# Kernel tuning notes

Measured on AMD Instinct MI355X. Metric: run time of the kernel, lower is better.

Reference implementation:

```python
import jax, jax.numpy as jnp
import numpy as np

E, H, I, B, K = 8, 2048, 5632, 1024, 2


def setup_inputs() -> dict:
    key = jax.random.key(0)
    k_x, k_id, k_w, k_g, k_u, k_d = jax.random.split(key, 6)
    x = jax.random.normal(k_x, (B, H), dtype=jnp.float32)
    expert_ids = jax.random.randint(k_id, (B, K), 0, E).astype(jnp.int32)
    ew = jax.random.uniform(k_w, (B, K), dtype=jnp.float32)
    expert_weights = ew / jnp.sum(ew, axis=-1, keepdims=True)  # router probs, sum to 1
    scale = 0.02
    gate_weights = jax.random.normal(k_g, (E, H, I), dtype=jnp.float32) * scale
    up_weights = jax.random.normal(k_u, (E, H, I), dtype=jnp.float32) * scale
    down_weights = jax.random.normal(k_d, (E, I, H), dtype=jnp.float32) * scale
    return {
        "x": x,
        "expert_ids": expert_ids,
        "expert_weights": expert_weights,
        "gate_weights": gate_weights,
        "up_weights": up_weights,
        "down_weights": down_weights,
    }


def reference(x, expert_ids, expert_weights, gate_weights, up_weights, down_weights):
    # Faithful math: per token t, expert e = expert_ids[t,k]:
    #   out[t] = sum_k expert_weights[t,k] * (silu(x W_gate_e) * (x W_up_e)) W_down_e
    # Implemented as dense all-expert GEMMs + select, which computes the
    # identical per-expert matmuls as the original's gathered-weight einsums
    # without materializing the [B,K,H,I] gathered weight tensor.
    gate_all = jnp.einsum('bh,ehi->bei', x, gate_weights)        # [B,E,I]
    up_all = jnp.einsum('bh,ehi->bei', x, up_weights)            # [B,E,I]
    act_all = jax.nn.silu(gate_all) * up_all                     # [B,E,I]
    out_all = jnp.einsum('bei,eih->beh', act_all, down_weights)  # [B,E,H]
    # Select the top_k experts' outputs per token: [B,K,H]
    sel = jnp.take_along_axis(out_all, expert_ids[:, :, None], axis=1)
    return jnp.sum(sel * expert_weights[:, :, None], axis=1)     # [B,H]
```

## Files before the change

### kernel.cpp

```cpp
#include <hip/hip_runtime.h>
#include <hip/hip_bf16.h>

#define E_ 8
#define H_ 2048
#define I_ 5632
#define B_ 1024
#define K_ 2
#define NROWS (B_*K_)

#define BM 128
#define BN 64
#define BK 64
#define MAXT 24
#define NKG (H_/BK)
#define NKD (I_/BK)
#define NYG (I_/BN)
#define NYD (H_/BN)

typedef __attribute__((ext_vector_type(8))) __bf16 bf16x8;
typedef __attribute__((ext_vector_type(4))) float f32x4;

union BF4 { __bf16 b[4]; uint2 q; };
union BF8 { __bf16 b[8]; uint4 q; };

__device__ __forceinline__ void gld_lds16(const void* g, void* l) {
  __builtin_amdgcn_global_load_lds(
      (const __attribute__((address_space(1))) void*)g,
      (__attribute__((address_space(3))) void*)l, 16, 0, 0);
}

#define GLOAD4(dst, ptr) asm volatile("global_load_dwordx4 %0, %1, off" : "=v"(dst) : "v"(ptr))
#define WAITV(N) do { asm volatile("s_waitcnt vmcnt(" #N ")" ::: "memory"); __builtin_amdgcn_sched_barrier(0); } while(0)
#define WAITL()  do { asm volatile("s_waitcnt lgkmcnt(0)" ::: "memory"); __builtin_amdgcn_sched_barrier(0); } while(0)
#define BAR()    __builtin_amdgcn_s_barrier()

#define MSK(c) (((c)&7) ^ (((c)>>2)&7))

__global__ void cvtx_kernel(const float* __restrict__ x, __bf16* __restrict__ xb) {
  int i = (blockIdx.x * 256 + threadIdx.x) * 8;
  float4 a = *(const float4*)(x + i);
  float4 b = *(const float4*)(x + i + 4);
  BF8 r;
  r.b[0] = (__bf16)a.x; r.b[1] = (__bf16)a.y; r.b[2] = (__bf16)a.z; r.b[3] = (__bf16)a.w;
  r.b[4] = (__bf16)b.x; r.b[5] = (__bf16)b.y; r.b[6] = (__bf16)b.z; r.b[7] = (__bf16)b.w;
  *(uint4*)(xb + i) = r.q;
}

__global__ void route_kernel(const int* __restrict__ ids,
                             int* __restrict__ counts, int* __restrict__ offsets,
                             int* __restrict__ tlist, int* __restrict__ row_of,
                             int* __restrict__ tile_e, int* __restrict__ tile_m) {
  __shared__ int sc[E_], sp[E_], so[E_];
  int t = threadIdx.x;
  if (t < E_) { sc[t] = 0; sp[t] = 0; }
  __syncthreads();
  for (int idx = t; idx < NROWS; idx += 256) atomicAdd(&sc[ids[idx]], 1);
  __syncthreads();
  if (t == 0) {
    int acc = 0;
    for (int e = 0; e < E_; ++e) { so[e] = acc; acc += sc[e]; }
    int nt = 0;
    for (int e = 0; e < E_; ++e)
      for (int m0 = 0; m0 < sc[e]; m0 += BM) { tile_e[nt] = e; tile_m[nt] = m0; ++nt; }
    for (; nt < MAXT; ++nt) { tile_e[nt] = 0; tile_m[nt] = 0x7FFFFFFF; }
  }
  __syncthreads();
  for (int idx = t; idx < NROWS; idx += 256) {
    int e = ids[idx];
    int slot = atomicAdd(&sp[e], 1);
    int row = so[e] + slot;
    tlist[row] = idx / K_;
    row_of[idx] = row;
  }
  if (t < E_) { counts[t] = sc[t]; offsets[t] = so[t]; }
}

__global__ __launch_bounds__(256, 3) void gateup_kernel(
    const __bf16* __restrict__ xb, const float* __restrict__ gw,
    const float* __restrict__ uw, const int* __restrict__ counts,
    const int* __restrict__ offsets, const int* __restrict__ tlist,
    const int* __restrict__ tile_e, const int* __restrict__ tile_m,
    __bf16* __restrict__ act)
{
  extern __shared__ char smem[];
  char* As0 = smem;
  char* As1 = smem + 16384;
  char* Bg  = smem + 32768;
  char* Bu  = smem + 40960;

  const int id = blockIdx.x;
  const int w  = (id & 7) * 264 + (id >> 3);
  const int tt = w % MAXT;
  const int ny = w / MAXT;
  const int e  = tile_e[tt];
  const int m0 = tile_m[tt];
  const int cnt = counts[e];
  if (m0 >= cnt) return;
  const int off = offsets[e];
  const int n0 = ny * BN;

  const int tid  = threadIdx.x;
  const int lane = tid & 63;
  const int wave = tid >> 6;
  const int wr = (wave >> 1) * 64;
  const int wc = (wave & 1) * 32;

  const __bf16* asrc0; const __bf16* asrc1; const __bf16* asrc2; const __bf16* asrc3;
  int ad0, ad1, ad2, ad3;
  {
    const __bf16* s[4]; int d[4];
#pragma unroll
    for (int i = 0; i < 4; ++i) {
      int f = i*256 + tid;
      int r = f >> 3, cs = f & 7;
      int rr = m0 + r; if (rr >= cnt) rr = cnt - 1;
      int tok = tlist[off + rr];
      s[i] = xb + (size_t)tok * H_ + ((cs ^ (r & 7)) << 3);
      d[i] = f * 16;
    }
    asrc0=s[0]; asrc1=s[1]; asrc2=s[2]; asrc3=s[3];
    ad0=d[0]; ad1=d[1]; ad2=d[2]; ad3=d[3];
  }

  const int cq = tid & 15;
  const int kb = (tid >> 4) * 4;
  const float* pg0 = gw + ((size_t)e*H_ + kb + 0)*I_ + n0 + 4*cq;
  const float* pg1 = gw + ((size_t)e*H_ + kb + 1)*I_ + n0 + 4*cq;
  const float* pg2 = gw + ((size_t)e*H_ + kb + 2)*I_ + n0 + 4*cq;
  const float* pg3 = gw + ((size_t)e*H_ + kb + 3)*I_ + n0 + 4*cq;
  const float* pu0 = uw + ((size_t)e*H_ + kb + 0)*I_ + n0 + 4*cq;
  const float* pu1 = uw + ((size_t)e*H_ + kb + 1)*I_ + n0 + 4*cq;
  const float* pu2 = uw + ((size_t)e*H_ + kb + 2)*I_ + n0 + 4*cq;
  const float* pu3 = uw + ((size_t)e*H_ + kb + 3)*I_ + n0 + 4*cq;
  const int slot = kb >> 3;
  const int half = (kb & 4) << 1;
  int bw0, bw1, bw2, bw3;
  {
    int b[4];
#pragma unroll
    for (int i = 0; i < 4; ++i) {
      int c = 4*cq + i;
      b[i] = c*128 + ((slot ^ MSK(c)) << 4) + half;
    }
    bw0=b[0]; bw1=b[1]; bw2=b[2]; bw3=b[3];
  }

  f32x4 vg_0,vg_1,vg_2,vg_3, vu_0,vu_1,vu_2,vu_3;

  f32x4 accg[4][2], accu[4][2];
#pragma unroll
  for (int i = 0; i < 4; ++i)
#pragma unroll
    for (int j = 0; j < 2; ++j) {
      accg[i][j] = (f32x4){0.f,0.f,0.f,0.f};
      accu[i][j] = (f32x4){0.f,0.f,0.f,0.f};
    }

  auto COMPUTE = [&](const char* Ab) {
    __builtin_amdgcn_s_setprio(1);
#pragma unroll
    for (int kk = 0; kk < 2; ++kk) {
      const int ks = kk*4 + (lane >> 4);
      const int r0 = wr + (lane & 15);
      const int swa = (ks ^ (r0 & 7)) << 4;
      bf16x8 a0 = *(const bf16x8*)(Ab + (r0 +  0)*128 + swa);
      bf16x8 a1 = *(const bf16x8*)(Ab + (r0 + 16)*128 + swa);
      bf16x8 a2 = *(const bf16x8*)(Ab + (r0 + 32)*128 + swa);
      bf16x8 a3 = *(const bf16x8*)(Ab + (r0 + 48)*128 + swa);
      const int c0 = wc + (lane & 15);
      const int swb0 = (ks ^ MSK(c0)) << 4;
      const int swb1 = swb0 ^ (4 << 4);
      bf16x8 g0 = *(const bf16x8*)(Bg + c0*128 + swb0);
      bf16x8 g1 = *(const bf16x8*)(Bg + (c0+16)*128 + swb1);
      bf16x8 u0 = *(const bf16x8*)(Bu + c0*128 + swb0);
      bf16x8 u1 = *(const bf16x8*)(Bu + (c0+16)*128 + swb1);
      accg[0][0] = __builtin_amdgcn_mfma_f32_16x16x32_bf16(a0, g0, accg[0][0], 0,0,0);
      accg[1][0] = __builtin_amdgcn_mfma_f32_16x16x32_bf16(a1, g0, accg[1][0], 0,0,0);
      accg[2][0] = __builtin_amdgcn_mfma_f32_16x16x32_bf16(a2, g0, accg[2][0], 0,0,0);
      accg[3][0] = __builtin_amdgcn_mfma_f32_16x16x32_bf16(a3, g0, accg[3][0], 0,0,0);
      accg[0][1] = __builtin_amdgcn_mfma_f32_16x16x32_bf16(a0, g1, accg[0][1], 0,0,0);
      accg[1][1] = __builtin_amdgcn_mfma_f32_16x16x32_bf16(a1, g1, accg[1][1], 0,0,0);
      accg[2][1] = __builtin_amdgcn_mfma_f32_16x16x32_bf16(a2, g1, accg[2][1], 0,0,0);
      accg[3][1] = __builtin_amdgcn_mfma_f32_16x16x32_bf16(a3, g1, accg[3][1], 0,0,0);
      accu[0][0] = __builtin_amdgcn_mfma_f32_16x16x32_bf16(a0, u0, accu[0][0], 0,0,0);
      accu[1][0] = __builtin_amdgcn_mfma_f32_16x16x32_bf16(a1, u0, accu[1][0], 0,0,0);
      accu[2][0] = __builtin_amdgcn_mfma_f32_16x16x32_bf16(a2, u0, accu[2][0], 0,0,0);
      accu[3][0] = __builtin_amdgcn_mfma_f32_16x16x32_bf16(a3, u0, accu[3][0], 0,0,0);
      accu[0][1] = __builtin_amdgcn_mfma_f32_16x16x32_bf16(a0, u1, accu[0][1], 0,0,0);
      accu[1][1] = __builtin_amdgcn_mfma_f32_16x16x32_bf16(a1, u1, accu[1][1], 0,0,0);
      accu[2][1] = __builtin_amdgcn_mfma_f32_16x16x32_bf16(a2, u1, accu[2][1], 0,0,0);
      accu[3][1] = __builtin_amdgcn_mfma_f32_16x16x32_bf16(a3, u1, accu[3][1], 0,0,0);
    }
    __builtin_amdgcn_s_setprio(0);
  };

#define GU_PF(KPF) do { size_t o_ = (size_t)(KPF)*(size_t)BK*(size_t)I_; \
    GLOAD4(vg_0, pg0+o_); GLOAD4(vu_0, pu0+o_); \
    GLOAD4(vg_1, pg1+o_); GLOAD4(vu_1, pu1+o_); \
    GLOAD4(vg_2, pg2+o_); GLOAD4(vu_2, pu2+o_); \
    GLOAD4(vg_3, pg3+o_); GLOAD4(vu_3, pu3+o_); } while(0)

#define GU_CVW1(BB, V0, V1, V2, V3, BWI, I) do { BF4 p_; \
    p_.b[0]=(__bf16)V0[I]; p_.b[1]=(__bf16)V1[I]; p_.b[2]=(__bf16)V2[I]; p_.b[3]=(__bf16)V3[I]; \
    *(uint2*)((BB)+BWI) = p_.q; } while(0)

#define GU_CVW() do { \
    GU_CVW1(Bg, vg_0, vg_1, vg_2, vg_3, bw0, 0); \
    GU_CVW1(Bg, vg_0, vg_1, vg_2, vg_3, bw1, 1); \
    GU_CVW1(Bg, vg_0, vg_1, vg_2, vg_3, bw2, 2); \
    GU_CVW1(Bg, vg_0, vg_1, vg_2, vg_3, bw3, 3); \
    GU_CVW1(Bu, vu_0, vu_1, vu_2, vu_3, bw0, 0); \
    GU_CVW1(Bu, vu_0, vu_1, vu_2, vu_3, bw1, 1); \
    GU_CVW1(Bu, vu_0, vu_1, vu_2, vu_3, bw2, 2); \
    GU_CVW1(Bu, vu_0, vu_1, vu_2, vu_3, bw3, 3); } while(0)

#define GU_GLDA(DST, KPF) do { size_t k_ = (size_t)(KPF)*(size_t)BK; \
    gld_lds16(asrc0 + k_, (DST)+ad0); gld_lds16(asrc1 + k_, (DST)+ad1); \
    gld_lds16(asrc2 + k_, (DST)+ad2); gld_lds16(asrc3 + k_, (DST)+ad3); } while(0)

  GU_PF(0);
  WAITV(0);
  GU_CVW();
  GU_GLDA(As0, 0);
  WAITV(0);
  GU_PF(1);
  GU_GLDA(As1, 1);
  WAITL();
  BAR();

#pragma unroll 1
  for (int kt = 0; kt < NKG; kt += 2) {
    {
      int kpf = kt + 2; if (kpf > NKG-1) kpf = NKG-1;
      COMPUTE(As0);
      WAITV(4);
      WAITL();
      BAR();
      GU_CVW();
      GU_PF(kpf);
      WAITV(8);
      WAITL();
      BAR();
      GU_GLDA(As0, kpf);
    }
    {
      int kpf = kt + 3; if (kpf > NKG-1) kpf = NKG-1;
      COMPUTE(As1);
      WAITV(4);
      WAITL();
      BAR();
      GU_CVW();
      GU_PF(kpf);
      WAITV(8);
      WAITL();
      BAR();
      GU_GLDA(As1, kpf);
    }
  }
  WAITV(0);
  WAITL();

  const int rsub = (lane >> 4) * 4;
  const int csub = lane & 15;
#pragma unroll
  for (int mi = 0; mi < 4; ++mi)
#pragma unroll
    for (int j = 0; j < 4; ++j) {
      int rl = wr + mi*16 + rsub + j;
      if (m0 + rl < cnt) {
        size_t orow = (size_t)(off + m0 + rl) * I_ + n0 + wc + csub;
#pragma unroll
        for (int cg = 0; cg < 2; ++cg) {
          float g = accg[mi][cg][j];
          float u = accu[mi][cg][j];
          float sg = g / (1.0f + __expf(-g));
          act[orow + cg*16] = (__bf16)(sg * u);
        }
      }
    }
#undef GU_PF
#undef GU_CVW
#undef GU_CVW1
#undef GU_GLDA
}

__global__ __launch_bounds__(256, 3) void down_kernel(
    const __bf16* __restrict__ act, const float* __restrict__ dw,
    const int* __restrict__ counts, const int* __restrict__ offsets,
    const int* __restrict__ tile_e, const int* __restrict__ tile_m,
    float* __restrict__ rowbuf)
{
  extern __shared__ char smem[];
  char* As0 = smem;
  char* As1 = smem + 16384;
  char* Bs0 = smem + 32768;
  char* Bs1 = smem + 40960;

  const int id = blockIdx.x;
  const int w  = (id & 7) * 96 + (id >> 3);
  const int tt = w % MAXT;
  const int ny = w / MAXT;
  const int e  = tile_e[tt];
  const int m0 = tile_m[tt];
  const int cnt = counts[e];
  if (m0 >= cnt) return;
  const int off = offsets[e];
  const int n0 = ny * BN;

  const int tid  = threadIdx.x;
  const int lane = tid & 63;
  const int wave = tid >> 6;
  const int wr = (wave >> 1) * 64;
  const int wc = (wave & 1) * 32;

  const __bf16* asrc0; const __bf16* asrc1; const __bf16* asrc2; const __bf16* asrc3;
  int ad0, ad1, ad2, ad3;
  {
    const __bf16* s[4]; int d[4];
#pragma unroll
    for (int i = 0; i < 4; ++i) {
      int f = i*256 + tid;
      int r = f >> 3, cs = f & 7;
      int rr = m0 + r; if (rr >= cnt) rr = cnt - 1;
      s[i] = act + (size_t)(off + rr) * I_ + ((cs ^ (r & 7)) << 3);
      d[i] = f * 16;
    }
    asrc0=s[0]; asrc1=s[1]; asrc2=s[2]; asrc3=s[3];
    ad0=d[0]; ad1=d[1]; ad2=d[2]; ad3=d[3];
  }

  const int cq = tid & 15;
  const int kb = (tid >> 4) * 4;
  const float* pd0 = dw + ((size_t)e*I_ + kb + 0)*H_ + n0 + 4*cq;
  const float* pd1 = dw + ((size_t)e*I_ + kb + 1)*H_ + n0 + 4*cq;
  const float* pd2 = dw + ((size_t)e*I_ + kb + 2)*H_ + n0 + 4*cq;
  const float* pd3 = dw + ((size_t)e*I_ + kb + 3)*H_ + n0 + 4*cq;
  const int slot = kb >> 3;
  const int half = (kb & 4) << 1;
  int bw0, bw1, bw2, bw3;
  {
    int b[4];
#pragma unroll
    for (int i = 0; i < 4; ++i) {
      int c = 4*cq + i;
      b[i] = c*128 + ((slot ^ MSK(c)) << 4) + half;
    }
    bw0=b[0]; bw1=b[1]; bw2=b[2]; bw3=b[3];
  }

  f32x4 vdA_0,vdA_1,vdA_2,vdA_3;
  f32x4 vdB_0,vdB_1,vdB_2,vdB_3;

  f32x4 acc[4][2];
#pragma unroll
  for (int i = 0; i < 4; ++i)
#pragma unroll
    for (int j = 0; j < 2; ++j) acc[i][j] = (f32x4){0.f,0.f,0.f,0.f};

  auto COMPUTE = [&](const char* Ab, const char* Bb) {
    __builtin_amdgcn_s_setprio(1);
#pragma unroll
    for (int kk = 0; kk < 2; ++kk) {
      const int ks = kk*4 + (lane >> 4);
      const int r0 = wr + (lane & 15);
      const int swa = (ks ^ (r0 & 7)) << 4;
      bf16x8 a0 = *(const bf16x8*)(Ab + (r0 +  0)*128 + swa);
      bf16x8 a1 = *(const bf16x8*)(Ab + (r0 + 16)*128 + swa);
      bf16x8 a2 = *(const bf16x8*)(Ab + (r0 + 32)*128 + swa);
      bf16x8 a3 = *(const bf16x8*)(Ab + (r0 + 48)*128 + swa);
      const int c0 = wc + (lane & 15);
      const int swb0 = (ks ^ MSK(c0)) << 4;
      const int swb1 = swb0 ^ (4 << 4);
      bf16x8 b0 = *(const bf16x8*)(Bb + c0*128 + swb0);
      bf16x8 b1 = *(const bf16x8*)(Bb + (c0+16)*128 + swb1);
      acc[0][0] = __builtin_amdgcn_mfma_f32_16x16x32_bf16(a0, b0, acc[0][0], 0,0,0);
      acc[1][0] = __builtin_amdgcn_mfma_f32_16x16x32_bf16(a1, b0, acc[1][0], 0,0,0);
      acc[2][0] = __builtin_amdgcn_mfma_f32_16x16x32_bf16(a2, b0, acc[2][0], 0,0,0);
      acc[3][0] = __builtin_amdgcn_mfma_f32_16x16x32_bf16(a3, b0, acc[3][0], 0,0,0);
      acc[0][1] = __builtin_amdgcn_mfma_f32_16x16x32_bf16(a0, b1, acc[0][1], 0,0,0);
      acc[1][1] = __builtin_amdgcn_mfma_f32_16x16x32_bf16(a1, b1, acc[1][1], 0,0,0);
      acc[2][1] = __builtin_amdgcn_mfma_f32_16x16x32_bf16(a2, b1, acc[2][1], 0,0,0);
      acc[3][1] = __builtin_amdgcn_mfma_f32_16x16x32_bf16(a3, b1, acc[3][1], 0,0,0);
    }
    __builtin_amdgcn_s_setprio(0);
  };

#define DN_PF(S, KPF) do { size_t o_ = (size_t)(KPF)*(size_t)BK*(size_t)H_; \
    GLOAD4(vd##S##_0, pd0+o_); GLOAD4(vd##S##_1, pd1+o_); \
    GLOAD4(vd##S##_2, pd2+o_); GLOAD4(vd##S##_3, pd3+o_); } while(0)

#define DN_CVW1(BB, V0, V1, V2, V3, BWI, I) do { BF4 p_; \
    p_.b[0]=(__bf16)V0[I]; p_.b[1]=(__bf16)V1[I]; p_.b[2]=(__bf16)V2[I]; p_.b[3]=(__bf16)V3[I]; \
    *(uint2*)((BB)+BWI) = p_.q; } while(0)

#define DN_CVW(S, BB) do { \
    DN_CVW1(BB, vd##S##_0, vd##S##_1, vd##S##_2, vd##S##_3, bw0, 0); \
    DN_CVW1(BB, vd##S##_0, vd##S##_1, vd##S##_2, vd##S##_3, bw1, 1); \
    DN_CVW1(BB, vd##S##_0, vd##S##_1, vd##S##_2, vd##S##_3, bw2, 2); \
    DN_CVW1(BB, vd##S##_0, vd##S##_1, vd##S##_2, vd##S##_3, bw3, 3); } while(0)

#define DN_GLDA(DST, KPF) do { size_t k_ = (size_t)(KPF)*(size_t)BK; \
    gld_lds16(asrc0 + k_, (DST)+ad0); gld_lds16(asrc1 + k_, (DST)+ad1); \
    gld_lds16(asrc2 + k_, (DST)+ad2); gld_lds16(asrc3 + k_, (DST)+ad3); } while(0)

  DN_PF(A, 0);
  DN_GLDA(As0, 0);
  WAITV(4);
  DN_CVW(A, Bs0);
  DN_PF(B, 1);
  DN_GLDA(As1, 1);
  WAITV(8);
  WAITL();
  BAR();

#pragma unroll 1
  for (int kt = 0; kt < NKD; kt += 2) {
    {
      int kpf = kt + 2; if (kpf > NKD-1) kpf = NKD-1;
      DN_PF(A, kpf);
      COMPUTE(As0, Bs0);
      WAITV(8);
      DN_CVW(B, Bs1);
      WAITV(4);
      WAITL();
      BAR();
      DN_GLDA(As0, kpf);
    }
    {
      int kpf = kt + 3; if (kpf > NKD-1) kpf = NKD-1;
      DN_PF(B, kpf);
      COMPUTE(As1, Bs1);
      WAITV(8);
      DN_CVW(A, Bs0);
      WAITV(4);
      WAITL();
      BAR();
      DN_GLDA(As1, kpf);
    }
  }
  WAITV(0);
  WAITL();

  const int rsub = (lane >> 4) * 4;
  const int csub = lane & 15;
#pragma unroll
  for (int mi = 0; mi < 4; ++mi)
#pragma unroll
    for (int j = 0; j < 4; ++j) {
      int rl = wr + mi*16 + rsub + j;
      if (m0 + rl < cnt) {
        size_t orow = (size_t)(off + m0 + rl) * H_ + n0 + wc + csub;
#pragma unroll
        for (int cg = 0; cg < 2; ++cg)
          rowbuf[orow + cg*16] = acc[mi][cg][j];
      }
    }
#undef DN_PF
#undef DN_CVW
#undef DN_CVW1
#undef DN_GLDA
}

__global__ void combine_kernel(const float* __restrict__ ew, const int* __restrict__ row_of,
                               const float* __restrict__ rowbuf, float* __restrict__ out) {
  int idx = blockIdx.x * 256 + threadIdx.x;
  int t  = idx >> 9;
  int h4 = idx & 511;
  float w0 = ew[t*2+0], w1 = ew[t*2+1];
  int r0 = row_of[t*2+0], r1 = row_of[t*2+1];
  float4 a = *(const float4*)(rowbuf + (size_t)r0*H_ + h4*4);
  float4 b = *(const float4*)(rowbuf + (size_t)r1*H_ + h4*4);
  float4 o;
  o.x = w0*a.x + w1*b.x; o.y = w0*a.y + w1*b.y;
  o.z = w0*a.z + w1*b.z; o.w = w0*a.w + w1*b.w;
  *(float4*)(out + (size_t)idx*4) = o;
}

extern "C" void kernel_launch(void* const* d_in, const int* in_sizes, int n_in,
                              void* d_out, int out_size, void* d_ws, size_t ws_size,
                              hipStream_t stream) {
  const float* x   = (const float*)d_in[0];
  const int*   ids = (const int*)d_in[1];
  const float* ew  = (const float*)d_in[2];
  const float* gw  = (const float*)d_in[3];
  const float* uw  = (const float*)d_in[4];
  const float* dwn = (const float*)d_in[5];
  float* out = (float*)d_out;

  char* ws = (char*)d_ws;
  int* counts  = (int*)ws;
  int* offsets = counts + 8;
  int* tlist   = offsets + 8;
  int* row_of  = tlist + NROWS;
  int* tile_e  = row_of + NROWS;
  int* tile_m  = tile_e + MAXT;
  __bf16* xb   = (__bf16*)(ws + 32768);
  __bf16* act  = (__bf16*)(ws + 32768 + (size_t)B_*H_*2);
  float* rowbuf = (float*)(ws + 32768 + (size_t)B_*H_*2 + (size_t)NROWS*I_*2);

  hipFuncSetAttribute(reinterpret_cast<const void*>(&gateup_kernel),
                      hipFuncAttributeMaxDynamicSharedMemorySize, 49152);
  hipFuncSetAttribute(reinterpret_cast<const void*>(&down_kernel),
                      hipFuncAttributeMaxDynamicSharedMemorySize, 49152);

  cvtx_kernel<<<B_*H_/(256*8), 256, 0, stream>>>(x, xb);
  route_kernel<<<1, 256, 0, stream>>>(ids, counts, offsets, tlist, row_of, tile_e, tile_m);

  gateup_kernel<<<MAXT*NYG, 256, 49152, stream>>>(xb, gw, uw, counts, offsets, tlist,
                                                  tile_e, tile_m, act);

  down_kernel<<<MAXT*NYD, 256, 49152, stream>>>(act, dwn, counts, offsets,
                                                tile_e, tile_m, rowbuf);

  combine_kernel<<<(B_*H_/4)/256, 256, 0, stream>>>(ew, row_of, rowbuf, out);
}
```

Measured before the change: 419.9 us.

## Widen gate/up tile to 128 columns with double-buffered B tiles and BK 32

```diff
diff --git a/kernel.cpp b/kernel.cpp
--- a/kernel.cpp
+++ b/kernel.cpp
@@ -9,12 +9,16 @@
 #define NROWS (B_*K_)
 
 #define BM 128
+#define MAXT 24
+
+#define GBN 128
+#define GBK 32
+#define NK2 (H_/GBK)
+#define NYG2 (I_/GBN)
+
 #define BN 64
 #define BK 64
-#define MAXT 24
-#define NKG (H_/BK)
 #define NKD (I_/BK)
-#define NYG (I_/BN)
 #define NYD (H_/BN)
 
 typedef __attribute__((ext_vector_type(8))) __bf16 bf16x8;
@@ -75,7 +79,7 @@
   if (t < E_) { counts[t] = sc[t]; offsets[t] = so[t]; }
 }
 
-__global__ __launch_bounds__(256, 3) void gateup_kernel(
+__global__ __launch_bounds__(256, 2) void gateup_kernel(
     const __bf16* __restrict__ xb, const float* __restrict__ gw,
     const float* __restrict__ uw, const int* __restrict__ counts,
     const int* __restrict__ offsets, const int* __restrict__ tlist,
@@ -84,12 +88,14 @@
 {
   extern __shared__ char smem[];
   char* As0 = smem;
-  char* As1 = smem + 16384;
-  char* Bg  = smem + 32768;
-  char* Bu  = smem + 40960;
+  char* As1 = smem + 8192;
+  char* Bg0 = smem + 16384;
+  char* Bu0 = smem + 24576;
+  char* Bg1 = smem + 32768;
+  char* Bu1 = smem + 40960;
 
   const int id = blockIdx.x;
-  const int w  = (id & 7) * 264 + (id >> 3);
+  const int w  = (id & 7) * 132 + (id >> 3);
   const int tt = w % MAXT;
   const int ny = w / MAXT;
   const int e  = tile_e[tt];
@@ -97,104 +103,116 @@
   const int cnt = counts[e];
   if (m0 >= cnt) return;
   const int off = offsets[e];
-  const int n0 = ny * BN;
+  const int n0 = ny * GBN;
 
   const int tid  = threadIdx.x;
   const int lane = tid & 63;
   const int wave = tid >> 6;
   const int wr = (wave >> 1) * 64;
-  const int wc = (wave & 1) * 32;
-
-  const __bf16* asrc0; const __bf16* asrc1; const __bf16* asrc2; const __bf16* asrc3;
-  int ad0, ad1, ad2, ad3;
+  const int wc = (wave & 1) * 64;
+
+  const __bf16* asrc0; const __bf16* asrc1;
+  int ad0, ad1;
   {
-    const __bf16* s[4]; int d[4];
-#pragma unroll
-    for (int i = 0; i < 4; ++i) {
-      int f = i*256 + tid;
-      int r = f >> 3, cs = f & 7;
+    const __bf16* s[2]; int d[2];
+#pragma unroll
+    for (int j = 0; j < 2; ++j) {
+      int g = j*256 + tid;
+      int ks = g >> 7;
+      int sl = g & 127;
+      int r  = sl ^ (ks << 2);
       int rr = m0 + r; if (rr >= cnt) rr = cnt - 1;
       int tok = tlist[off + rr];
-      s[i] = xb + (size_t)tok * H_ + ((cs ^ (r & 7)) << 3);
-      d[i] = f * 16;
-    }
-    asrc0=s[0]; asrc1=s[1]; asrc2=s[2]; asrc3=s[3];
-    ad0=d[0]; ad1=d[1]; ad2=d[2]; ad3=d[3];
-  }
-
-  const int cq = tid & 15;
-  const int kb = (tid >> 4) * 4;
-  const float* pg0 = gw + ((size_t)e*H_ + kb + 0)*I_ + n0 + 4*cq;
-  const float* pg1 = gw + ((size_t)e*H_ + kb + 1)*I_ + n0 + 4*cq;
-  const float* pg2 = gw + ((size_t)e*H_ + kb + 2)*I_ + n0 + 4*cq;
-  const float* pg3 = gw + ((size_t)e*H_ + kb + 3)*I_ + n0 + 4*cq;
-  const float* pu0 = uw + ((size_t)e*H_ + kb + 0)*I_ + n0 + 4*cq;
-  const float* pu1 = uw + ((size_t)e*H_ + kb + 1)*I_ + n0 + 4*cq;
-  const float* pu2 = uw + ((size_t)e*H_ + kb + 2)*I_ + n0 + 4*cq;
-  const float* pu3 = uw + ((size_t)e*H_ + kb + 3)*I_ + n0 + 4*cq;
-  const int slot = kb >> 3;
-  const int half = (kb & 4) << 1;
+      s[j] = xb + (size_t)tok * H_ + ks*8;
+      d[j] = g * 16;
+    }
+    asrc0=s[0]; asrc1=s[1]; ad0=d[0]; ad1=d[1];
+  }
+
+  const int q  = tid & 31;
+  const int kb = (tid >> 5) * 4;
+  const float* pg0 = gw + ((size_t)e*H_ + kb + 0)*I_ + n0 + 4*q;
+  const float* pg1 = gw + ((size_t)e*H_ + kb + 1)*I_ + n0 + 4*q;
+  const float* pg2 = gw + ((size_t)e*H_ + kb + 2)*I_ + n0 + 4*q;
+  const float* pg3 = gw + ((size_t)e*H_ + kb + 3)*I_ + n0 + 4*q;
+  const float* pu0 = uw + ((size_t)e*H_ + kb + 0)*I_ + n0 + 4*q;
+  const float* pu1 = uw + ((size_t)e*H_ + kb + 1)*I_ + n0 + 4*q;
+  const float* pu2 = uw + ((size_t)e*H_ + kb + 2)*I_ + n0 + 4*q;
+  const float* pu3 = uw + ((size_t)e*H_ + kb + 3)*I_ + n0 + 4*q;
   int bw0, bw1, bw2, bw3;
   {
+    int ksw  = kb >> 3;
+    int half = (kb & 4) << 1;
     int b[4];
 #pragma unroll
     for (int i = 0; i < 4; ++i) {
-      int c = 4*cq + i;
-      b[i] = c*128 + ((slot ^ MSK(c)) << 4) + half;
+      int slot = (q ^ (i << 2)) + (i << 5);
+      b[i] = ksw*2048 + slot*16 + half;
     }
     bw0=b[0]; bw1=b[1]; bw2=b[2]; bw3=b[3];
   }
 
+  const int ks = lane >> 4;
+  int aofs0;
+  int bofs0, bofs1, bofs2, bofs3;
+  {
+    int r0 = wr + (lane & 15);
+    aofs0 = ks*2048 + ((r0 ^ (ks << 2)) << 4);
+    int c0 = wc + (lane & 15);
+    int ii = c0 & 3;
+    int bb[4];
+#pragma unroll
+    for (int ni = 0; ni < 4; ++ni) {
+      int qq = (c0 >> 2) + ni*4;
+      int slot = (qq ^ (ii << 2)) + (ii << 5);
+      bb[ni] = ks*2048 + slot*16;
+    }
+    bofs0=bb[0]; bofs1=bb[1]; bofs2=bb[2]; bofs3=bb[3];
+  }
+
   f32x4 vg_0,vg_1,vg_2,vg_3, vu_0,vu_1,vu_2,vu_3;
 
-  f32x4 accg[4][2], accu[4][2];
+  f32x4 accg[4][4], accu[4][4];
 #pragma unroll
   for (int i = 0; i < 4; ++i)
 #pragma unroll
-    for (int j = 0; j < 2; ++j) {
+    for (int j = 0; j < 4; ++j) {
       accg[i][j] = (f32x4){0.f,0.f,0.f,0.f};
       accu[i][j] = (f32x4){0.f,0.f,0.f,0.f};
     }
 
-  auto COMPUTE = [&](const char* Ab) {
+  auto COMPUTE = [&](const char* Ap, const char* Bgp, const char* Bup) {
     __builtin_amdgcn_s_setprio(1);
-#pragma unroll
-    for (int kk = 0; kk < 2; ++kk) {
-      const int ks = kk*4 + (lane >> 4);
-      const int r0 = wr + (lane & 15);
-      const int swa = (ks ^ (r0 & 7)) << 4;
-      bf16x8 a0 = *(const bf16x8*)(Ab + (r0 +  0)*128 + swa);
-      bf16x8 a1 = *(const bf16x8*)(Ab + (r0 + 16)*128 + swa);
-      bf16x8 a2 = *(const bf16x8*)(Ab + (r0 + 32)*128 + swa);
-      bf16x8 a3 = *(const bf16x8*)(Ab + (r0 + 48)*128 + swa);
-      const int c0 = wc + (lane & 15);
-      const int swb0 = (ks ^ MSK(c0)) << 4;
-      const int swb1 = swb0 ^ (4 << 4);
-      bf16x8 g0 = *(const bf16x8*)(Bg + c0*128 + swb0);
-      bf16x8 g1 = *(const bf16x8*)(Bg + (c0+16)*128 + swb1);
-      bf16x8 u0 = *(const bf16x8*)(Bu + c0*128 + swb0);
-      bf16x8 u1 = *(const bf16x8*)(Bu + (c0+16)*128 + swb1);
-      accg[0][0] = __builtin_amdgcn_mfma_f32_16x16x32_bf16(a0, g0, accg[0][0], 0,0,0);
-      accg[1][0] = __builtin_amdgcn_mfma_f32_16x16x32_bf16(a1, g0, accg[1][0], 0,0,0);
-      accg[2][0] = __builtin_amdgcn_mfma_f32_16x16x32_bf16(a2, g0, accg[2][0], 0,0,0);
-      accg[3][0] = __builtin_amdgcn_mfma_f32_16x16x32_bf16(a3, g0, accg[3][0], 0,0,0);
-      accg[0][1] = __builtin_amdgcn_mfma_f32_16x16x32_bf16(a0, g1, accg[0][1], 0,0,0);
-      accg[1][1] = __builtin_amdgcn_mfma_f32_16x16x32_bf16(a1, g1, accg[1][1], 0,0,0);
-      accg[2][1] = __builtin_amdgcn_mfma_f32_16x16x32_bf16(a2, g1, accg[2][1], 0,0,0);
-      accg[3][1] = __builtin_amdgcn_mfma_f32_16x16x32_bf16(a3, g1, accg[3][1], 0,0,0);
-      accu[0][0] = __builtin_amdgcn_mfma_f32_16x16x32_bf16(a0, u0, accu[0][0], 0,0,0);
-      accu[1][0] = __builtin_amdgcn_mfma_f32_16x16x32_bf16(a1, u0, accu[1][0], 0,0,0);
-      accu[2][0] = __builtin_amdgcn_mfma_f32_16x16x32_bf16(a2, u0, accu[2][0], 0,0,0);
-      accu[3][0] = __builtin_amdgcn_mfma_f32_16x16x32_bf16(a3, u0, accu[3][0], 0,0,0);
-      accu[0][1] = __builtin_amdgcn_mfma_f32_16x16x32_bf16(a0, u1, accu[0][1], 0,0,0);
-      accu[1][1] = __builtin_amdgcn_mfma_f32_16x16x32_bf16(a1, u1, accu[1][1], 0,0,0);
-      accu[2][1] = __builtin_amdgcn_mfma_f32_16x16x32_bf16(a2, u1, accu[2][1], 0,0,0);
-      accu[3][1] = __builtin_amdgcn_mfma_f32_16x16x32_bf16(a3, u1, accu[3][1], 0,0,0);
-    }
+    bf16x8 a0 = *(const bf16x8*)(Ap + aofs0 + 0*256);
+    bf16x8 a1 = *(const bf16x8*)(Ap + aofs0 + 1*256);
+    bf16x8 a2 = *(const bf16x8*)(Ap + aofs0 + 2*256);
+    bf16x8 a3 = *(const bf16x8*)(Ap + aofs0 + 3*256);
+#define MM(ACC, A, B) ACC = __builtin_amdgcn_mfma_f32_16x16x32_bf16(A, B, ACC, 0,0,0)
+    {
+      bf16x8 b0 = *(const bf16x8*)(Bgp + bofs0);
+      bf16x8 b1 = *(const bf16x8*)(Bgp + bofs1);
+      bf16x8 b2 = *(const bf16x8*)(Bgp + bofs2);
+      bf16x8 b3 = *(const bf16x8*)(Bgp + bofs3);
+      MM(accg[0][0], a0, b0); MM(accg[1][0], a1, b0); MM(accg[2][0], a2, b0); MM(accg[3][0], a3, b0);
+      MM(accg[0][1], a0, b1); MM(accg[1][1], a1, b1); MM(accg[2][1], a2, b1); MM(accg[3][1], a3, b1);
+      MM(accg[0][2], a0, b2); MM(accg[1][2], a1, b2); MM(accg[2][2], a2, b2); MM(accg[3][2], a3, b2);
+      MM(accg[0][3], a0, b3); MM(accg[1][3], a1, b3); MM(accg[2][3], a2, b3); MM(accg[3][3], a3, b3);
+    }
+    {
+      bf16x8 b0 = *(const bf16x8*)(Bup + bofs0);
+      bf16x8 b1 = *(const bf16x8*)(Bup + bofs1);
+      bf16x8 b2 = *(const bf16x8*)(Bup + bofs2);
+      bf16x8 b3 = *(const bf16x8*)(Bup + bofs3);
+      MM(accu[0][0], a0, b0); MM(accu[1][0], a1, b0); MM(accu[2][0], a2, b0); MM(accu[3][0], a3, b0);
+      MM(accu[0][1], a0, b1); MM(accu[1][1], a1, b1); MM(accu[2][1], a2, b1); MM(accu[3][1], a3, b1);
+      MM(accu[0][2], a0, b2); MM(accu[1][2], a1, b2); MM(accu[2][2], a2, b2); MM(accu[3][2], a3, b2);
+      MM(accu[0][3], a0, b3); MM(accu[1][3], a1, b3); MM(accu[2][3], a2, b3); MM(accu[3][3], a3, b3);
+    }
+#undef MM
     __builtin_amdgcn_s_setprio(0);
   };
 
-#define GU_PF(KPF) do { size_t o_ = (size_t)(KPF)*(size_t)BK*(size_t)I_; \
+#define GU_PF(KPF) do { size_t o_ = (size_t)(KPF)*(size_t)GBK*(size_t)I_; \
     GLOAD4(vg_0, pg0+o_); GLOAD4(vu_0, pu0+o_); \
     GLOAD4(vg_1, pg1+o_); GLOAD4(vu_1, pu1+o_); \
     GLOAD4(vg_2, pg2+o_); GLOAD4(vu_2, pu2+o_); \
@@ -204,39 +222,36 @@
     p_.b[0]=(__bf16)V0[I]; p_.b[1]=(__bf16)V1[I]; p_.b[2]=(__bf16)V2[I]; p_.b[3]=(__bf16)V3[I]; \
     *(uint2*)((BB)+BWI) = p_.q; } while(0)
 
-#define GU_CVW() do { \
-    GU_CVW1(Bg, vg_0, vg_1, vg_2, vg_3, bw0, 0); \
-    GU_CVW1(Bg, vg_0, vg_1, vg_2, vg_3, bw1, 1); \
-    GU_CVW1(Bg, vg_0, vg_1, vg_2, vg_3, bw2, 2); \
-    GU_CVW1(Bg, vg_0, vg_1, vg_2, vg_3, bw3, 3); \
-    GU_CVW1(Bu, vu_0, vu_1, vu_2, vu_3, bw0, 0); \
-    GU_CVW1(Bu, vu_0, vu_1, vu_2, vu_3, bw1, 1); \
-    GU_CVW1(Bu, vu_0, vu_1, vu_2, vu_3, bw2, 2); \
-    GU_CVW1(Bu, vu_0, vu_1, vu_2, vu_3, bw3, 3); } while(0)
-
-#define GU_GLDA(DST, KPF) do { size_t k_ = (size_t)(KPF)*(size_t)BK; \
-    gld_lds16(asrc0 + k_, (DST)+ad0); gld_lds16(asrc1 + k_, (DST)+ad1); \
-    gld_lds16(asrc2 + k_, (DST)+ad2); gld_lds16(asrc3 + k_, (DST)+ad3); } while(0)
+#define GU_CVW(BG, BU) do { \
+    GU_CVW1(BG, vg_0, vg_1, vg_2, vg_3, bw0, 0); \
+    GU_CVW1(BG, vg_0, vg_1, vg_2, vg_3, bw1, 1); \
+    GU_CVW1(BG, vg_0, vg_1, vg_2, vg_3, bw2, 2); \
+    GU_CVW1(BG, vg_0, vg_1, vg_2, vg_3, bw3, 3); \
+    GU_CVW1(BU, vu_0, vu_1, vu_2, vu_3, bw0, 0); \
+    GU_CVW1(BU, vu_0, vu_1, vu_2, vu_3, bw1, 1); \
+    GU_CVW1(BU, vu_0, vu_1, vu_2, vu_3, bw2, 2); \
+    GU_CVW1(BU, vu_0, vu_1, vu_2, vu_3, bw3, 3); } while(0)
+
+#define GU_GLDA(DST, KPF) do { size_t k_ = (size_t)(KPF)*(size_t)GBK; \
+    gld_lds16(asrc0 + k_, (DST)+ad0); gld_lds16(asrc1 + k_, (DST)+ad1); } while(0)
 
   GU_PF(0);
   WAITV(0);
-  GU_CVW();
+  GU_CVW(Bg0, Bu0);
   GU_GLDA(As0, 0);
-  WAITV(0);
   GU_PF(1);
+  WAITV(8);
   GU_GLDA(As1, 1);
   WAITL();
   BAR();
 
 #pragma unroll 1
-  for (int kt = 0; kt < NKG; kt += 2) {
+  for (int kt = 0; kt < NK2; kt += 2) {
     {
-      int kpf = kt + 2; if (kpf > NKG-1) kpf = NKG-1;
-      COMPUTE(As0);
-      WAITV(4);
-      WAITL();
-      BAR();
-      GU_CVW();
+      int kpf = kt + 2; if (kpf > NK2-1) kpf = NK2-1;
+      COMPUTE(As0, Bg0, Bu0);
+      WAITV(1);
+      GU_CVW(Bg1, Bu1);
       GU_PF(kpf);
       WAITV(8);
       WAITL();
@@ -244,12 +259,10 @@
       GU_GLDA(As0, kpf);
     }
     {
-      int kpf = kt + 3; if (kpf > NKG-1) kpf = NKG-1;
-      COMPUTE(As1);
-      WAITV(4);
-      WAITL();
-      BAR();
-      GU_CVW();
+      int kpf = kt + 3; if (kpf > NK2-1) kpf = NK2-1;
+      COMPUTE(As1, Bg1, Bu1);
+      WAITV(1);
+      GU_CVW(Bg0, Bu0);
       GU_PF(kpf);
       WAITV(8);
       WAITL();
@@ -270,11 +283,11 @@
       if (m0 + rl < cnt) {
         size_t orow = (size_t)(off + m0 + rl) * I_ + n0 + wc + csub;
 #pragma unroll
-        for (int cg = 0; cg < 2; ++cg) {
-          float g = accg[mi][cg][j];
-          float u = accu[mi][cg][j];
+        for (int ni = 0; ni < 4; ++ni) {
+          float g = accg[mi][ni][j];
+          float u = accu[mi][ni][j];
           float sg = g / (1.0f + __expf(-g));
-          act[orow + cg*16] = (__bf16)(sg * u);
+          act[orow + ni*16] = (__bf16)(sg * u);
         }
       }
     }
@@ -506,8 +519,8 @@
   cvtx_kernel<<<B_*H_/(256*8), 256, 0, stream>>>(x, xb);
   route_kernel<<<1, 256, 0, stream>>>(ids, counts, offsets, tlist, row_of, tile_e, tile_m);
 
-  gateup_kernel<<<MAXT*NYG, 256, 49152, stream>>>(xb, gw, uw, counts, offsets, tlist,
-                                                  tile_e, tile_m, act);
+  gateup_kernel<<<MAXT*NYG2, 256, 49152, stream>>>(xb, gw, uw, counts, offsets, tlist,
+                                                   tile_e, tile_m, act);
 
   down_kernel<<<MAXT*NYD, 256, 49152, stream>>>(act, dwn, counts, offsets,
                                                 tile_e, tile_m, rowbuf);
```

Result: slower. 438.0 us (+4.3%).
